# Kernel optimization log

Measured on AMD Instinct MI355X. Metric: run time of the kernel, lower is better.

The kernel has to match this reference:

```python
import jax, jax.numpy as jnp
import numpy as np

N, E = 100000, 1600000
F_IN, H, HG, L, C = 128, 128, 128, 3, 40


def setup_inputs() -> dict:
    key = jax.random.key(0)
    ks = jax.random.split(key, 12)
    s = 0.05
    return dict(
        x=jax.random.normal(ks[0], (N, F_IN), jnp.float32),
        edge_index=jax.random.randint(ks[1], (2, E), 0, N),
        edge_weight=jax.random.uniform(ks[2], (E,), jnp.float32),
        h0=jax.random.normal(ks[3], (N, HG), jnp.float32),
        linW=jax.random.normal(ks[4], (F_IN, H), jnp.float32) * s,
        linB=jnp.zeros((H,), jnp.float32),
        convW=jax.random.normal(ks[5], (L, H, H), jnp.float32) * s,
        convB=jnp.zeros((L, H), jnp.float32),
        gru_Wih=jax.random.normal(ks[6], (3 * HG, H), jnp.float32) * s,
        gru_Whh=jax.random.normal(ks[7], (3 * HG, HG), jnp.float32) * s,
        gru_bih=jnp.zeros((3 * HG,), jnp.float32),
        gru_bhh=jnp.zeros((3 * HG,), jnp.float32),
        fcW=jax.random.normal(ks[8], (HG, C), jnp.float32) * s,
        fcB=jnp.zeros((C,), jnp.float32),
    )


def _gru(x, h, Wih, Whh, bih, bhh):
    # torch.nn.GRUCell math (gate order: r, z, n)
    gi = x @ Wih.T + bih  # [N, 3*HG]
    gh = h @ Whh.T + bhh  # [N, 3*HG]
    ir, iz, in_ = jnp.split(gi, 3, axis=-1)
    hr, hz, hn = jnp.split(gh, 3, axis=-1)
    r = jax.nn.sigmoid(ir + hr)
    z = jax.nn.sigmoid(iz + hz)
    n = jnp.tanh(in_ + r * hn)
    return (1.0 - z) * n + z * h


def _gcn_conv(x, src, dst, ew, W, b, n_nodes):
    # PyG GCNConv: linear -> symmetric-normalized sparse aggregation -> bias
    xw = x @ W  # [N, H]
    deg = jax.ops.segment_sum(ew, dst, num_segments=n_nodes)
    dinv = jnp.where(deg > 0, jax.lax.rsqrt(deg), 0.0)
    norm = dinv[src] * ew * dinv[dst]  # [E+N]
    msg = xw[src] * norm[:, None]      # gather + scale (irregular access)
    out = jax.ops.segment_sum(msg, dst, num_segments=n_nodes)  # scatter-add
    return out + b


def reference(x, edge_index, edge_weight, h0, linW, linB, convW, convB,
              gru_Wih, gru_Whh, gru_bih, gru_bhh, fcW, fcB):
    n_nodes = x.shape[0]
    # GCNConv default: add self-loops with weight 1 before normalization
    loops = jnp.arange(n_nodes)
    src = jnp.concatenate([edge_index[0], loops])
    dst = jnp.concatenate([edge_index[1], loops])
    ew = jnp.concatenate([edge_weight, jnp.ones((n_nodes,), edge_weight.dtype)])

    h = h0
    xh = jax.nn.relu(x @ linW + linB)
    h = _gru(xh, h, gru_Wih, gru_Whh, gru_bih, gru_bhh)
    for l in range(convW.shape[0]):  # fixed small layer count
        xh = jax.nn.relu(_gcn_conv(xh, src, dst, ew, convW[l], convB[l], n_nodes))
        h = _gru(xh, h, gru_Wih, gru_Whh, gru_bih, gru_bhh)
    return h @ fcW + fcB
```

## Files before the change

### kernel.cpp

```cpp
#include <hip/hip_runtime.h>
#include <hip/hip_bf16.h>
#include <math.h>

typedef __attribute__((ext_vector_type(8))) short bf8_t;
typedef __attribute__((ext_vector_type(4))) float f4_t;
typedef __attribute__((ext_vector_type(8))) unsigned short us8_t;

__device__ inline unsigned short f2bf(float f) {
  union { float f; unsigned u; } x; x.f = f;
  unsigned r = x.u + 0x7FFF + ((x.u >> 16) & 1);
  return (unsigned short)(r >> 16);
}
__device__ inline float bflo(unsigned v) {
  union { unsigned u; float f; } x; x.u = v << 16; return x.f;
}
__device__ inline float bfhi(unsigned v) {
  union { unsigned u; float f; } x; x.u = v & 0xFFFF0000u; return x.f;
}

__device__ inline void async_copy16(const void* g, void* l) {
  __builtin_amdgcn_global_load_lds(
      (const __attribute__((address_space(1))) unsigned int*)g,
      (__attribute__((address_space(3))) unsigned int*)l, 16, 0, 0);
}


__device__ inline void packB_body(const float* __restrict__ W,
                                  unsigned short* __restrict__ out,
                                  int K, int Ncols, int ldw, int trans, int bid) {
  int idx = bid * 256 + threadIdx.x;
  int total = (Ncols / 16) * (K / 32) * 64;
  if (idx >= total) return;
  int lane = idx & 63;
  int frag = idx >> 6;
  int kt = K / 32;
  int k0 = frag % kt;
  int n0 = frag / kt;
  int n = n0 * 16 + (lane & 15);
  int kbase = k0 * 32 + (lane >> 4) * 8;
  us8_t v;
#pragma unroll
  for (int j = 0; j < 8; ++j) {
    int k = kbase + j;
    float f = trans ? W[(size_t)n * ldw + k] : W[(size_t)k * ldw + n];
    v[j] = f2bf(f);
  }
  *(us8_t*)(out + (size_t)idx * 8) = v;
}

__device__ inline void fill_body(const int* __restrict__ src, const int* __restrict__ dst,
                                 const float* __restrict__ ew, const int* __restrict__ rowptr,
                                 const int* __restrict__ pos, int2* __restrict__ csr,
                                 int E, int bid) {
  int e = bid * 256 + threadIdx.x;
  if (e >= E) return;
  int d = dst[e];
  int p = rowptr[d] + pos[e];
  unsigned long long v = (unsigned long long)(unsigned)src[e] |
                         ((unsigned long long)(unsigned)__float_as_int(ew[e]) << 32);
  __builtin_nontemporal_store(v, (unsigned long long*)(csr + p));
}

__device__ inline void deg_body(const int* __restrict__ rowptr, const int2* __restrict__ csr,
                                float* __restrict__ dinv, int N, int bid) {
  int n = bid * 256 + threadIdx.x;
  if (n >= N) return;
  int b = rowptr[n], e = rowptr[n + 1];
  float s = 1.0f;
  for (int j = b; j < e; ++j) {
    unsigned long long v = __builtin_nontemporal_load((const unsigned long long*)(csr + j));
    s += __int_as_float((int)(v >> 32));
  }
  dinv[n] = rsqrtf(s);
}

__device__ inline void norm_body(const int* __restrict__ rowptr, int2* __restrict__ csr,
                                 const float* __restrict__ dinv, int N, int bid) {
  int n = bid * 256 + threadIdx.x;
  if (n >= N) return;
  int b = rowptr[n], e = rowptr[n + 1];
  float dn = dinv[n];
  for (int j = b; j < e; ++j) {
    unsigned long long v = __builtin_nontemporal_load((const unsigned long long*)(csr + j));
    int s = (int)v;
    float w = dinv[s] * __int_as_float((int)(v >> 32)) * dn;
    unsigned long long nv = (unsigned long long)(unsigned)s |
                            ((unsigned long long)(unsigned)__float_as_int(w) << 32);
    __builtin_nontemporal_store(nv, (unsigned long long*)(csr + j));
  }
}

__device__ inline void gemm_body(const unsigned short* __restrict__ A,
                                 const unsigned short* __restrict__ Bp,
                                 const float* __restrict__ bias,
                                 unsigned short* __restrict__ C, int M, int bid,
                                 bool relu, bool hasbias, unsigned char* smem) {
  int wave = threadIdx.x >> 6, lane = threadIdx.x & 63;
  int row0 = (bid * 4 + wave) * 16;
  int m = lane & 15, q = lane >> 4;

#pragma unroll
  for (int i = 0; i < 8; ++i) {
    int f = wave * 8 + i;
    async_copy16((const unsigned char*)Bp + (size_t)f * 1024 + lane * 16,
                 smem + f * 1024);
  }
  __syncthreads();
  if (row0 >= M) return;

  int arow = row0 + m; if (arow >= M) arow = M - 1;
  bf8_t a[4];
#pragma unroll
  for (int k0 = 0; k0 < 4; ++k0)
    a[k0] = *(const bf8_t*)(A + (size_t)arow * 128 + k0 * 32 + q * 8);

#pragma unroll
  for (int n0 = 0; n0 < 8; ++n0) {
    f4_t acc = {};
#pragma unroll
    for (int k0 = 0; k0 < 4; ++k0) {
      bf8_t b = *(const bf8_t*)(smem + (n0 * 4 + k0) * 1024 + lane * 16);
      acc = __builtin_amdgcn_mfma_f32_16x16x32_bf16(a[k0], b, acc, 0, 0, 0);
    }
    int col = n0 * 16 + m;
    float bs = hasbias ? bias[col] : 0.f;
#pragma unroll
    for (int r = 0; r < 4; ++r) {
      int grow = row0 + q * 4 + r;
      if (grow < M) {
        float v = acc[r] + bs;
        if (relu) v = fmaxf(v, 0.f);
        C[(size_t)grow * 128 + col] = f2bf(v);
      }
    }
  }
}

__device__ inline void gru_stage(const unsigned short* __restrict__ Bi,
                                 const unsigned short* __restrict__ Bh,
                                 unsigned char* smem, int wave, int lane, int g) {
#pragma unroll
  for (int s = 0; s < 6; ++s) {
    int cc = g + 8 * (s >= 3 ? s - 3 : s);
    const unsigned short* src = (s < 3) ? Bi : Bh;
    int f = s * 4 + wave;
    async_copy16((const unsigned char*)src + ((size_t)(cc * 4 + wave)) * 1024 + lane * 16,
                 smem + f * 1024);
  }
}

__device__ inline void gru_core(const bf8_t* ax, const float* h_in, float* h_out,
                                const unsigned short* __restrict__ Bi,
                                const unsigned short* __restrict__ Bh,
                                const float* __restrict__ bih, const float* __restrict__ bhh,
                                int M, int row0, int wave, int lane, unsigned char* smem) {
  int m = lane & 15, q = lane >> 4;
  int arow = row0 + m; if (arow >= M) arow = M - 1;

  bf8_t ah[4];
#pragma unroll
  for (int k0 = 0; k0 < 4; ++k0) {
    const float* hp = h_in + (size_t)arow * 128 + k0 * 32 + q * 8;
    float4 h0 = *(const float4*)hp;
    float4 h1 = *(const float4*)(hp + 4);
    bf8_t t;
    t[0] = (short)f2bf(h0.x); t[1] = (short)f2bf(h0.y);
    t[2] = (short)f2bf(h0.z); t[3] = (short)f2bf(h0.w);
    t[4] = (short)f2bf(h1.x); t[5] = (short)f2bf(h1.y);
    t[6] = (short)f2bf(h1.z); t[7] = (short)f2bf(h1.w);
    ah[k0] = t;
  }

  for (int g = 0; g < 8; ++g) {
    __syncthreads();
    f4_t air = {}, aiz = {}, ain = {}, ahr = {}, ahz = {}, ahn = {};
#pragma unroll
    for (int k0 = 0; k0 < 4; ++k0) {
      bf8_t br = *(const bf8_t*)(smem + (0 * 4 + k0) * 1024 + lane * 16);
      bf8_t bz = *(const bf8_t*)(smem + (1 * 4 + k0) * 1024 + lane * 16);
      bf8_t bn = *(const bf8_t*)(smem + (2 * 4 + k0) * 1024 + lane * 16);
      bf8_t cr = *(const bf8_t*)(smem + (3 * 4 + k0) * 1024 + lane * 16);
      bf8_t cz = *(const bf8_t*)(smem + (4 * 4 + k0) * 1024 + lane * 16);
      bf8_t cn = *(const bf8_t*)(smem + (5 * 4 + k0) * 1024 + lane * 16);
      air = __builtin_amdgcn_mfma_f32_16x16x32_bf16(ax[k0], br, air, 0, 0, 0);
      aiz = __builtin_amdgcn_mfma_f32_16x16x32_bf16(ax[k0], bz, aiz, 0, 0, 0);
      ain = __builtin_amdgcn_mfma_f32_16x16x32_bf16(ax[k0], bn, ain, 0, 0, 0);
      ahr = __builtin_amdgcn_mfma_f32_16x16x32_bf16(ah[k0], cr, ahr, 0, 0, 0);
      ahz = __builtin_amdgcn_mfma_f32_16x16x32_bf16(ah[k0], cz, ahz, 0, 0, 0);
      ahn = __builtin_amdgcn_mfma_f32_16x16x32_bf16(ah[k0], cn, ahn, 0, 0, 0);
    }
    __syncthreads();
    if (g < 7) gru_stage(Bi, Bh, smem, wave, lane, g + 1);

    int col = g * 16 + m;
    float bir_ = bih[col], biz_ = bih[col + 128], bin_ = bih[col + 256];
    float bhr_ = bhh[col], bhz_ = bhh[col + 128], bhn_ = bhh[col + 256];
#pragma unroll
    for (int r = 0; r < 4; ++r) {
      int grow = row0 + q * 4 + r;
      if (grow < M) {
        float hprev = h_in[(size_t)grow * 128 + col];
        float rr = 1.f / (1.f + expf(-(air[r] + bir_ + ahr[r] + bhr_)));
        float zz = 1.f / (1.f + expf(-(aiz[r] + biz_ + ahz[r] + bhz_)));
        float nn = tanhf(ain[r] + bin_ + rr * (ahn[r] + bhn_));
        h_out[(size_t)grow * 128 + col] = (1.f - zz) * nn + zz * hprev;
      }
    }
  }
}

__device__ inline void gru_body(const unsigned short* __restrict__ xh,
                                const float* h_in, float* h_out,
                                const unsigned short* __restrict__ Bi,
                                const unsigned short* __restrict__ Bh,
                                const float* __restrict__ bih, const float* __restrict__ bhh,
                                int M, int bid, unsigned char* smem) {
  int wave = threadIdx.x >> 6, lane = threadIdx.x & 63;
  int row0 = (bid * 4 + wave) * 16;
  gru_stage(Bi, Bh, smem, wave, lane, 0);
  int m = lane & 15, q = lane >> 4;
  int arow = row0 + m; if (arow >= M) arow = M - 1;
  bf8_t ax[4];
#pragma unroll
  for (int k0 = 0; k0 < 4; ++k0)
    ax[k0] = *(const bf8_t*)(xh + (size_t)arow * 128 + k0 * 32 + q * 8);
  gru_core(ax, h_in, h_out, Bi, Bh, bih, bhh, M, row0, wave, lane, smem);
}


__global__ __launch_bounds__(256) void k_prep(
    const float* __restrict__ linW, const float* __restrict__ convW,
    const float* __restrict__ Wih, const float* __restrict__ Whh,
    unsigned short* __restrict__ linWp, unsigned short* __restrict__ convWp,
    unsigned short* __restrict__ Bi, unsigned short* __restrict__ Bh,
    int* __restrict__ cnt, int N) {
  int b = blockIdx.x;
  if (b < 8)  { packB_body(linW, linWp, 128, 128, 128, 0, b); return; }
  if (b < 32) { int l = (b - 8) >> 3;
                packB_body(convW + (size_t)l * 16384, convWp + (size_t)l * 16384,
                           128, 128, 128, 0, (b - 8) & 7); return; }
  if (b < 56) { packB_body(Wih, Bi, 128, 384, 128, 1, b - 32); return; }
  if (b < 80) { packB_body(Whh, Bh, 128, 384, 128, 1, b - 56); return; }
  int i = (b - 80) * 256 + threadIdx.x;
  if (i < N) cnt[i] = 0;
}

__global__ __launch_bounds__(256) void k_count_f2bf(
    const int* __restrict__ dst, int* __restrict__ cnt, int* __restrict__ pos, int E,
    const float* __restrict__ xin, unsigned short* __restrict__ xout, size_t n8,
    int nCnt) {
  if ((int)blockIdx.x < nCnt) {
    int e = blockIdx.x * 256 + threadIdx.x;
    if (e < E) pos[e] = atomicAdd(&cnt[dst[e]], 1);
    return;
  }
  size_t i = (size_t)(blockIdx.x - nCnt) * 256 + threadIdx.x;
  if (i >= n8) return;
  const float4* p = (const float4*)(xin + i * 8);
  float4 a = p[0], b = p[1];
  us8_t v;
  v[0] = f2bf(a.x); v[1] = f2bf(a.y); v[2] = f2bf(a.z); v[3] = f2bf(a.w);
  v[4] = f2bf(b.x); v[5] = f2bf(b.y); v[6] = f2bf(b.z); v[7] = f2bf(b.w);
  *(us8_t*)(xout + i * 8) = v;
}

__global__ __launch_bounds__(256) void k_scan_block(
    const int* __restrict__ cnt, int* __restrict__ partial,
    int* __restrict__ bsum, int n) {
  __shared__ int s[256];
  int tid = threadIdx.x;
  int i = blockIdx.x * 256 + tid;
  s[tid] = (i < n) ? cnt[i] : 0;
  __syncthreads();
#pragma unroll
  for (int d = 1; d < 256; d <<= 1) {
    int t = (tid >= d) ? s[tid - d] : 0;
    __syncthreads();
    s[tid] += t;
    __syncthreads();
  }
  if (i < n) partial[i] = s[tid];
  if (tid == 255) bsum[blockIdx.x] = s[255];
}

__global__ __launch_bounds__(512) void k_scan_sums(int* __restrict__ bsum, int nb) {
  __shared__ int s[512];
  int tid = threadIdx.x;
  s[tid] = (tid < nb) ? bsum[tid] : 0;
  __syncthreads();
#pragma unroll
  for (int d = 1; d < 512; d <<= 1) {
    int t = (tid >= d) ? s[tid - d] : 0;
    __syncthreads();
    s[tid] += t;
    __syncthreads();
  }
  if (tid < nb) bsum[tid] = s[tid];
}

__global__ __launch_bounds__(256) void k_scan_add(
    const int* __restrict__ partial, const int* __restrict__ bsum,
    int* __restrict__ rowptr, int n) {
  int i = blockIdx.x * 256 + threadIdx.x;
  if (i == 0) rowptr[0] = 0;
  if (i < n) {
    int v = partial[i] + (blockIdx.x > 0 ? bsum[blockIdx.x - 1] : 0);
    rowptr[i + 1] = v;
  }
}

__global__ __launch_bounds__(256) void k_fill_lin(
    const int* __restrict__ src, const int* __restrict__ dstI,
    const float* __restrict__ ew, const int* __restrict__ rowptr,
    const int* __restrict__ pos, int2* __restrict__ csr, int E,
    const unsigned short* __restrict__ A, const unsigned short* __restrict__ Bp,
    const float* __restrict__ bias, unsigned short* __restrict__ C, int M,
    int nFill) {
  __shared__ unsigned char smem[32 * 1024];
  if ((int)blockIdx.x < nFill) {
    fill_body(src, dstI, ew, rowptr, pos, csr, E, blockIdx.x);
    return;
  }
  gemm_body(A, Bp, bias, C, M, blockIdx.x - nFill, true, true, smem);
}

__global__ __launch_bounds__(256) void k_deg_gru(
    const int* __restrict__ rowptr, const int2* __restrict__ csr,
    float* __restrict__ dinv, int N,
    const unsigned short* __restrict__ xh, const float* h_in, float* h_out,
    const unsigned short* __restrict__ Bi, const unsigned short* __restrict__ Bh,
    const float* __restrict__ bih, const float* __restrict__ bhh, int M,
    int nDeg) {
  __shared__ unsigned char smem[24 * 1024];
  if ((int)blockIdx.x < nDeg) {
    deg_body(rowptr, csr, dinv, N, blockIdx.x);
    return;
  }
  gru_body(xh, h_in, h_out, Bi, Bh, bih, bhh, M, blockIdx.x - nDeg, smem);
}

__global__ __launch_bounds__(256) void k_norm_conv(
    const int* __restrict__ rowptr, int2* __restrict__ csr,
    const float* __restrict__ dinv, int N,
    const unsigned short* __restrict__ A, const unsigned short* __restrict__ Bp,
    unsigned short* __restrict__ C, int M, int nNorm) {
  __shared__ unsigned char smem[32 * 1024];
  if ((int)blockIdx.x < nNorm) {
    norm_body(rowptr, csr, dinv, N, blockIdx.x);
    return;
  }
  gemm_body(A, Bp, nullptr, C, M, blockIdx.x - nNorm, false, false, smem);
}

__global__ __launch_bounds__(256) void k_gru_conv(
    const unsigned short* __restrict__ xh, const float* h_in, float* h_out,
    const unsigned short* __restrict__ Bi, const unsigned short* __restrict__ Bh,
    const float* __restrict__ bih, const float* __restrict__ bhh,
    const unsigned short* __restrict__ Bp, unsigned short* __restrict__ xw,
    int M, int nGru) {
  __shared__ unsigned char smem[32 * 1024];
  if ((int)blockIdx.x < nGru) {
    gru_body(xh, h_in, h_out, Bi, Bh, bih, bhh, M, blockIdx.x, smem);
    return;
  }
  gemm_body(xh, Bp, nullptr, xw, M, blockIdx.x - nGru, false, false, smem);
}

__global__ __launch_bounds__(256) void k_gru(
    const unsigned short* __restrict__ xh, const float* h_in, float* h_out,
    const unsigned short* __restrict__ Bi, const unsigned short* __restrict__ Bh,
    const float* __restrict__ bih, const float* __restrict__ bhh, int M) {
  __shared__ unsigned char smem[24 * 1024];
  gru_body(xh, h_in, h_out, Bi, Bh, bih, bhh, M, blockIdx.x, smem);
}


__global__ __launch_bounds__(256) void k_gather(
    const int* __restrict__ rowptr, const int2* __restrict__ csr,
    const unsigned* __restrict__ xw,
    const float* __restrict__ dinv, const float* __restrict__ bias,
    unsigned* __restrict__ out, int N) {
  int wave = threadIdx.x >> 6;
  int lane = threadIdx.x & 63;
  int node = __builtin_amdgcn_readfirstlane(blockIdx.x * 4 + wave);
  if (node >= N) return;
  int beg = __builtin_amdgcn_readfirstlane(rowptr[node]);
  int end = __builtin_amdgcn_readfirstlane(rowptr[node + 1]);

  float accl = 0.f, acch = 0.f;
  int k = beg;
  for (; k + 4 <= end; k += 4) {
    unsigned long long r0 = __builtin_nontemporal_load((const unsigned long long*)(csr + k));
    unsigned long long r1 = __builtin_nontemporal_load((const unsigned long long*)(csr + k + 1));
    unsigned long long r2 = __builtin_nontemporal_load((const unsigned long long*)(csr + k + 2));
    unsigned long long r3 = __builtin_nontemporal_load((const unsigned long long*)(csr + k + 3));
    unsigned v0 = xw[((size_t)(unsigned)r0 << 6) + lane];
    unsigned v1 = xw[((size_t)(unsigned)r1 << 6) + lane];
    unsigned v2 = xw[((size_t)(unsigned)r2 << 6) + lane];
    unsigned v3 = xw[((size_t)(unsigned)r3 << 6) + lane];
    float w0 = __int_as_float((int)(r0 >> 32)), w1 = __int_as_float((int)(r1 >> 32));
    float w2 = __int_as_float((int)(r2 >> 32)), w3 = __int_as_float((int)(r3 >> 32));
    accl += bflo(v0) * w0; acch += bfhi(v0) * w0;
    accl += bflo(v1) * w1; acch += bfhi(v1) * w1;
    accl += bflo(v2) * w2; acch += bfhi(v2) * w2;
    accl += bflo(v3) * w3; acch += bfhi(v3) * w3;
  }
  for (; k < end; ++k) {
    unsigned long long r = __builtin_nontemporal_load((const unsigned long long*)(csr + k));
    unsigned v = xw[((size_t)(unsigned)r << 6) + lane];
    float w = __int_as_float((int)(r >> 32));
    accl += bflo(v) * w; acch += bfhi(v) * w;
  }

  float di = dinv[node];
  float sn = di * di;
  unsigned vs = xw[((size_t)node << 6) + lane];
  float2 b = *(const float2*)(bias + lane * 2);
  float rl = fmaxf(accl + bflo(vs) * sn + b.x, 0.f);
  float rh = fmaxf(acch + bfhi(vs) * sn + b.y, 0.f);
  unsigned o = (unsigned)f2bf(rl) | ((unsigned)f2bf(rh) << 16);
  out[((size_t)node << 6) + lane] = o;
}


template<bool RELU, bool BIAS>
__global__ __launch_bounds__(256) void k_gemm128(
    const float* __restrict__ A, const float* __restrict__ B,
    const float* __restrict__ bias, float* __restrict__ C, int M, int Nc) {
  __shared__ float As[64][36];
  __shared__ float Bs[32][64];
  int tid = threadIdx.x;
  int tx = tid & 15, ty = tid >> 4;
  int row0 = blockIdx.y * 64, col0 = blockIdx.x * 64;
  float acc[4][4] = {};

  for (int k0 = 0; k0 < 128; k0 += 32) {
#pragma unroll
    for (int i = 0; i < 2; ++i) {
      int f = tid + i * 256;
      int r = f >> 3, c4 = f & 7;
      int gr = row0 + r;
      float4 v = make_float4(0.f, 0.f, 0.f, 0.f);
      if (gr < M) v = *(const float4*)(A + (size_t)gr * 128 + k0 + c4 * 4);
      *(float4*)(&As[r][c4 * 4]) = v;
    }
#pragma unroll
    for (int i = 0; i < 2; ++i) {
      int f = tid + i * 256;
      int r = f >> 4, c4 = f & 15;
      int gc = col0 + c4 * 4;
      float4 v = make_float4(0.f, 0.f, 0.f, 0.f);
      if (gc + 3 < Nc) v = *(const float4*)(B + (size_t)(k0 + r) * Nc + gc);
      *(float4*)(&Bs[r][c4 * 4]) = v;
    }
    __syncthreads();
#pragma unroll
    for (int kk = 0; kk < 32; ++kk) {
      float4 b = *(float4*)(&Bs[kk][tx * 4]);
      float a0 = As[ty * 4 + 0][kk];
      float a1 = As[ty * 4 + 1][kk];
      float a2 = As[ty * 4 + 2][kk];
      float a3 = As[ty * 4 + 3][kk];
      acc[0][0] += a0 * b.x; acc[0][1] += a0 * b.y; acc[0][2] += a0 * b.z; acc[0][3] += a0 * b.w;
      acc[1][0] += a1 * b.x; acc[1][1] += a1 * b.y; acc[1][2] += a1 * b.z; acc[1][3] += a1 * b.w;
      acc[2][0] += a2 * b.x; acc[2][1] += a2 * b.y; acc[2][2] += a2 * b.z; acc[2][3] += a2 * b.w;
      acc[3][0] += a3 * b.x; acc[3][1] += a3 * b.y; acc[3][2] += a3 * b.z; acc[3][3] += a3 * b.w;
    }
    __syncthreads();
  }

#pragma unroll
  for (int i = 0; i < 4; ++i) {
    int gr = row0 + ty * 4 + i;
    if (gr >= M) continue;
#pragma unroll
    for (int j = 0; j < 4; ++j) {
      int gc = col0 + tx * 4 + j;
      if (gc >= Nc) continue;
      float v = acc[i][j];
      if (BIAS) v += bias[gc];
      if (RELU) v = fmaxf(v, 0.f);
      C[(size_t)gr * Nc + gc] = v;
    }
  }
}


extern "C" void kernel_launch(void* const* d_in, const int* in_sizes, int n_in,
                              void* d_out, int out_size, void* d_ws, size_t ws_size,
                              hipStream_t stream) {
  const float* x    = (const float*)d_in[0];
  const int*   ei   = (const int*)d_in[1];
  const float* ew   = (const float*)d_in[2];
  const float* h0   = (const float*)d_in[3];
  const float* linW = (const float*)d_in[4];
  const float* linB = (const float*)d_in[5];
  const float* convW= (const float*)d_in[6];
  const float* convB= (const float*)d_in[7];
  const float* Wih  = (const float*)d_in[8];
  const float* Whh  = (const float*)d_in[9];
  const float* bih  = (const float*)d_in[10];
  const float* bhh  = (const float*)d_in[11];
  const float* fcW  = (const float*)d_in[12];
  const float* fcB  = (const float*)d_in[13];

  int N = in_sizes[0] / 128;
  int E = in_sizes[1] / 2;
  const int* srcI = ei;
  const int* dstI = ei + E;
  int nb = (N + 255) / 256;

  float* ws = (float*)d_ws;
  size_t off = 0;
  float* dinv = ws + off; off += (size_t)N;
  if (off & 1) off++;
  float* h    = ws + off; off += (size_t)N * 128;
  int* iws = (int*)(ws + off);
  size_t ioff = 0;
  int2* csr    = (int2*)iws; ioff += (size_t)2 * E;
  int* cnt     = iws + ioff; ioff += (size_t)N;
  int* partial = iws + ioff; ioff += (size_t)N;
  int* bsum    = iws + ioff; ioff += 512;
  int* rowptr  = iws + ioff; ioff += (size_t)N + 1;
  ioff = (ioff + 3) & ~(size_t)3;
  unsigned short* usws = (unsigned short*)(iws + ioff);
  size_t uoff = 0;
  unsigned short* x_bf   = usws + uoff; uoff += (size_t)N * 128;
  unsigned short* xh_bf  = usws + uoff; uoff += (size_t)N * 128;
  unsigned short* xw_bf  = usws + uoff; uoff += (size_t)N * 128;
  unsigned short* linWp  = usws + uoff; uoff += 128 * 128;
  unsigned short* convWp = usws + uoff; uoff += 3 * 128 * 128;
  unsigned short* Bi     = usws + uoff; uoff += 384 * 128;
  unsigned short* Bh     = usws + uoff; uoff += 384 * 128;

  int* pos = (int*)xw_bf;

  int gwave = (N + 63) / 64;
  int nCnt  = (E + 255) / 256;
  int nF2   = (int)(((size_t)N * 16 + 255) / 256);

  k_prep<<<80 + nb, 256, 0, stream>>>(linW, convW, Wih, Whh,
                                      linWp, convWp, Bi, Bh, cnt, N);
  k_count_f2bf<<<nCnt + nF2, 256, 0, stream>>>(dstI, cnt, pos, E,
                                               x, x_bf, (size_t)N * 16, nCnt);
  k_scan_block<<<nb, 256, 0, stream>>>(cnt, partial, bsum, N);
  k_scan_sums<<<1, 512, 0, stream>>>(bsum, nb);
  k_scan_add<<<nb, 256, 0, stream>>>(partial, bsum, rowptr, N);
  k_fill_lin<<<nCnt + gwave, 256, 0, stream>>>(srcI, dstI, ew, rowptr, pos, csr, E,
                                               x_bf, linWp, linB, xh_bf, N, nCnt);
  k_deg_gru<<<nb + gwave, 256, 0, stream>>>(rowptr, csr, dinv, N,
                                            xh_bf, h0, h, Bi, Bh, bih, bhh, N, nb);
  k_norm_conv<<<nb + gwave, 256, 0, stream>>>(rowptr, csr, dinv, N,
                                              xh_bf, convWp, xw_bf, N, nb);

  int ggat = (N + 3) / 4;
  k_gather<<<ggat, 256, 0, stream>>>(rowptr, csr, (const unsigned*)xw_bf, dinv,
                                     convB, (unsigned*)xh_bf, N);
  k_gru_conv<<<2 * gwave, 256, 0, stream>>>(
      xh_bf, h, h, Bi, Bh, bih, bhh,
      convWp + (size_t)1 * 128 * 128, xw_bf, N, gwave);
  k_gather<<<ggat, 256, 0, stream>>>(rowptr, csr, (const unsigned*)xw_bf, dinv,
                                     convB + 128, (unsigned*)xh_bf, N);
  k_gru_conv<<<2 * gwave, 256, 0, stream>>>(
      xh_bf, h, h, Bi, Bh, bih, bhh,
      convWp + (size_t)2 * 128 * 128, xw_bf, N, gwave);
  k_gather<<<ggat, 256, 0, stream>>>(rowptr, csr, (const unsigned*)xw_bf, dinv,
                                     convB + 256, (unsigned*)xh_bf, N);
  k_gru<<<gwave, 256, 0, stream>>>(xh_bf, h, h, Bi, Bh, bih, bhh, N);
  dim3 g40(1, (N + 63) / 64);
  k_gemm128<false, true><<<g40, 256, 0, stream>>>(h, fcW, fcB, (float*)d_out, N, 40);
}
```

Baseline: 976.9 us.

## Use 512-thread blocks for fused GEMM/GRU kernels and fast sigmoid/tanh

The fused fill/deg/norm and GEMM/GRU kernels move from 256 to 512 threads per block, so each block covers 128 rows. The LDS weight staging is then split across 8 waves, which halves the per-block copy work and the number of redundant weight loads across the grid. The GRU gate math now uses __expf plus a hardware reciprocal instead of expf, 1/x and tanhf, trading some accuracy for fewer instructions. Larger blocks and launch_bounds(512,4) may also change register allocation and occupancy.

```diff
diff --git a/kernel.cpp b/kernel.cpp
--- a/kernel.cpp
+++ b/kernel.cpp
@@ -16,6 +16,12 @@
 }
 __device__ inline float bfhi(unsigned v) {
   union { unsigned u; float f; } x; x.u = v & 0xFFFF0000u; return x.f;
+}
+__device__ inline float fast_sig(float x) {
+  return __builtin_amdgcn_rcpf(1.f + __expf(-x));
+}
+__device__ inline float fast_tanh(float x) {
+  return 1.f - 2.f * __builtin_amdgcn_rcpf(1.f + __expf(2.f * x));
 }
 
 __device__ inline void async_copy16(const void* g, void* l) {
@@ -52,7 +58,7 @@
                                  const float* __restrict__ ew, const int* __restrict__ rowptr,
                                  const int* __restrict__ pos, int2* __restrict__ csr,
                                  int E, int bid) {
-  int e = bid * 256 + threadIdx.x;
+  int e = bid * 512 + threadIdx.x;
   if (e >= E) return;
   int d = dst[e];
   int p = rowptr[d] + pos[e];
@@ -63,7 +69,7 @@
 
 __device__ inline void deg_body(const int* __restrict__ rowptr, const int2* __restrict__ csr,
                                 float* __restrict__ dinv, int N, int bid) {
-  int n = bid * 256 + threadIdx.x;
+  int n = bid * 512 + threadIdx.x;
   if (n >= N) return;
   int b = rowptr[n], e = rowptr[n + 1];
   float s = 1.0f;
@@ -76,7 +82,7 @@
 
 __device__ inline void norm_body(const int* __restrict__ rowptr, int2* __restrict__ csr,
                                  const float* __restrict__ dinv, int N, int bid) {
-  int n = bid * 256 + threadIdx.x;
+  int n = bid * 512 + threadIdx.x;
   if (n >= N) return;
   int b = rowptr[n], e = rowptr[n + 1];
   float dn = dinv[n];
@@ -90,18 +96,18 @@
   }
 }
 
-__device__ inline void gemm_body(const unsigned short* __restrict__ A,
-                                 const unsigned short* __restrict__ Bp,
-                                 const float* __restrict__ bias,
-                                 unsigned short* __restrict__ C, int M, int bid,
-                                 bool relu, bool hasbias, unsigned char* smem) {
+__device__ inline void gemm_body8(const unsigned short* __restrict__ A,
+                                  const unsigned short* __restrict__ Bp,
+                                  const float* __restrict__ bias,
+                                  unsigned short* __restrict__ C, int M, int bid,
+                                  bool relu, bool hasbias, unsigned char* smem) {
   int wave = threadIdx.x >> 6, lane = threadIdx.x & 63;
-  int row0 = (bid * 4 + wave) * 16;
+  int row0 = (bid * 8 + wave) * 16;
   int m = lane & 15, q = lane >> 4;
 
 #pragma unroll
-  for (int i = 0; i < 8; ++i) {
-    int f = wave * 8 + i;
+  for (int i = 0; i < 4; ++i) {
+    int f = wave * 4 + i;
     async_copy16((const unsigned char*)Bp + (size_t)f * 1024 + lane * 16,
                  smem + f * 1024);
   }
@@ -136,15 +142,16 @@
   }
 }
 
-__device__ inline void gru_stage(const unsigned short* __restrict__ Bi,
-                                 const unsigned short* __restrict__ Bh,
-                                 unsigned char* smem, int wave, int lane, int g) {
-#pragma unroll
-  for (int s = 0; s < 6; ++s) {
+__device__ inline void gru_stage8(const unsigned short* __restrict__ Bi,
+                                  const unsigned short* __restrict__ Bh,
+                                  unsigned char* smem, int wave, int lane, int g) {
+#pragma unroll
+  for (int i = 0; i < 3; ++i) {
+    int f = wave * 3 + i;
+    int s = f >> 2, k0 = f & 3;
     int cc = g + 8 * (s >= 3 ? s - 3 : s);
     const unsigned short* src = (s < 3) ? Bi : Bh;
-    int f = s * 4 + wave;
-    async_copy16((const unsigned char*)src + ((size_t)(cc * 4 + wave)) * 1024 + lane * 16,
+    async_copy16((const unsigned char*)src + ((size_t)(cc * 4 + k0)) * 1024 + lane * 16,
                  smem + f * 1024);
   }
 }
@@ -190,7 +197,7 @@
       ahn = __builtin_amdgcn_mfma_f32_16x16x32_bf16(ah[k0], cn, ahn, 0, 0, 0);
     }
     __syncthreads();
-    if (g < 7) gru_stage(Bi, Bh, smem, wave, lane, g + 1);
+    if (g < 7) gru_stage8(Bi, Bh, smem, wave, lane, g + 1);
 
     int col = g * 16 + m;
     float bir_ = bih[col], biz_ = bih[col + 128], bin_ = bih[col + 256];
@@ -200,24 +207,24 @@
       int grow = row0 + q * 4 + r;
       if (grow < M) {
         float hprev = h_in[(size_t)grow * 128 + col];
-        float rr = 1.f / (1.f + expf(-(air[r] + bir_ + ahr[r] + bhr_)));
-        float zz = 1.f / (1.f + expf(-(aiz[r] + biz_ + ahz[r] + bhz_)));
-        float nn = tanhf(ain[r] + bin_ + rr * (ahn[r] + bhn_));
+        float rr = fast_sig(air[r] + bir_ + ahr[r] + bhr_);
+        float zz = fast_sig(aiz[r] + biz_ + ahz[r] + bhz_);
+        float nn = fast_tanh(ain[r] + bin_ + rr * (ahn[r] + bhn_));
         h_out[(size_t)grow * 128 + col] = (1.f - zz) * nn + zz * hprev;
       }
     }
   }
 }
 
-__device__ inline void gru_body(const unsigned short* __restrict__ xh,
-                                const float* h_in, float* h_out,
-                                const unsigned short* __restrict__ Bi,
-                                const unsigned short* __restrict__ Bh,
-                                const float* __restrict__ bih, const float* __restrict__ bhh,
-                                int M, int bid, unsigned char* smem) {
+__device__ inline void gru_body8(const unsigned short* __restrict__ xh,
+                                 const float* h_in, float* h_out,
+                                 const unsigned short* __restrict__ Bi,
+                                 const unsigned short* __restrict__ Bh,
+                                 const float* __restrict__ bih, const float* __restrict__ bhh,
+                                 int M, int bid, unsigned char* smem) {
   int wave = threadIdx.x >> 6, lane = threadIdx.x & 63;
-  int row0 = (bid * 4 + wave) * 16;
-  gru_stage(Bi, Bh, smem, wave, lane, 0);
+  int row0 = (bid * 8 + wave) * 16;
+  gru_stage8(Bi, Bh, smem, wave, lane, 0);
   int m = lane & 15, q = lane >> 4;
   int arow = row0 + m; if (arow >= M) arow = M - 1;
   bf8_t ax[4];
@@ -309,7 +316,7 @@
   }
 }
 
-__global__ __launch_bounds__(256) void k_fill_lin(
+__global__ __launch_bounds__(512, 4) void k_fill_lin(
     const int* __restrict__ src, const int* __restrict__ dstI,
     const float* __restrict__ ew, const int* __restrict__ rowptr,
     const int* __restrict__ pos, int2* __restrict__ csr, int E,
@@ -321,10 +328,10 @@
     fill_body(src, dstI, ew, rowptr, pos, csr, E, blockIdx.x);
     return;
   }
-  gemm_body(A, Bp, bias, C, M, blockIdx.x - nFill, true, true, smem);
-}
-
-__global__ __launch_bounds__(256) void k_deg_gru(
+  gemm_body8(A, Bp, bias, C, M, blockIdx.x - nFill, true, true, smem);
+}
+
+__global__ __launch_bounds__(512, 4) void k_deg_gru(
     const int* __restrict__ rowptr, const int2* __restrict__ csr,
     float* __restrict__ dinv, int N,
     const unsigned short* __restrict__ xh, const float* h_in, float* h_out,
@@ -336,10 +343,10 @@
     deg_body(rowptr, csr, dinv, N, blockIdx.x);
     return;
   }
-  gru_body(xh, h_in, h_out, Bi, Bh, bih, bhh, M, blockIdx.x - nDeg, smem);
-}
-
-__global__ __launch_bounds__(256) void k_norm_conv(
+  gru_body8(xh, h_in, h_out, Bi, Bh, bih, bhh, M, blockIdx.x - nDeg, smem);
+}
+
+__global__ __launch_bounds__(512, 4) void k_norm_conv(
     const int* __restrict__ rowptr, int2* __restrict__ csr,
     const float* __restrict__ dinv, int N,
     const unsigned short* __restrict__ A, const unsigned short* __restrict__ Bp,
@@ -349,10 +356,10 @@
     norm_body(rowptr, csr, dinv, N, blockIdx.x);
     return;
   }
-  gemm_body(A, Bp, nullptr, C, M, blockIdx.x - nNorm, false, false, smem);
-}
-
-__global__ __launch_bounds__(256) void k_gru_conv(
+  gemm_body8(A, Bp, nullptr, C, M, blockIdx.x - nNorm, false, false, smem);
+}
+
+__global__ __launch_bounds__(512, 4) void k_gru_conv(
     const unsigned short* __restrict__ xh, const float* h_in, float* h_out,
     const unsigned short* __restrict__ Bi, const unsigned short* __restrict__ Bh,
     const float* __restrict__ bih, const float* __restrict__ bhh,
@@ -360,18 +367,18 @@
     int M, int nGru) {
   __shared__ unsigned char smem[32 * 1024];
   if ((int)blockIdx.x < nGru) {
-    gru_body(xh, h_in, h_out, Bi, Bh, bih, bhh, M, blockIdx.x, smem);
+    gru_body8(xh, h_in, h_out, Bi, Bh, bih, bhh, M, blockIdx.x, smem);
     return;
   }
-  gemm_body(xh, Bp, nullptr, xw, M, blockIdx.x - nGru, false, false, smem);
-}
-
-__global__ __launch_bounds__(256) void k_gru(
+  gemm_body8(xh, Bp, nullptr, xw, M, blockIdx.x - nGru, false, false, smem);
+}
+
+__global__ __launch_bounds__(512, 4) void k_gru(
     const unsigned short* __restrict__ xh, const float* h_in, float* h_out,
     const unsigned short* __restrict__ Bi, const unsigned short* __restrict__ Bh,
     const float* __restrict__ bih, const float* __restrict__ bhh, int M) {
   __shared__ unsigned char smem[24 * 1024];
-  gru_body(xh, h_in, h_out, Bi, Bh, bih, bhh, M, blockIdx.x, smem);
+  gru_body8(xh, h_in, h_out, Bi, Bh, bih, bhh, M, blockIdx.x, smem);
 }
 
 
@@ -535,9 +542,11 @@
 
   int* pos = (int*)xw_bf;
 
-  int gwave = (N + 63) / 64;
-  int nCnt  = (E + 255) / 256;
-  int nF2   = (int)(((size_t)N * 16 + 255) / 256);
+  int gw8  = (N + 127) / 128;
+  int nCnt = (E + 255) / 256;
+  int nF2  = (int)(((size_t)N * 16 + 255) / 256);
+  int n512 = (N + 511) / 512;
+  int e512 = (E + 511) / 512;
 
   k_prep<<<80 + nb, 256, 0, stream>>>(linW, convW, Wih, Whh,
                                       linWp, convWp, Bi, Bh, cnt, N);
@@ -546,27 +555,27 @@
   k_scan_block<<<nb, 256, 0, stream>>>(cnt, partial, bsum, N);
   k_scan_sums<<<1, 512, 0, stream>>>(bsum, nb);
   k_scan_add<<<nb, 256, 0, stream>>>(partial, bsum, rowptr, N);
-  k_fill_lin<<<nCnt + gwave, 256, 0, stream>>>(srcI, dstI, ew, rowptr, pos, csr, E,
-                                               x_bf, linWp, linB, xh_bf, N, nCnt);
-  k_deg_gru<<<nb + gwave, 256, 0, stream>>>(rowptr, csr, dinv, N,
-                                            xh_bf, h0, h, Bi, Bh, bih, bhh, N, nb);
-  k_norm_conv<<<nb + gwave, 256, 0, stream>>>(rowptr, csr, dinv, N,
-                                              xh_bf, convWp, xw_bf, N, nb);
+  k_fill_lin<<<e512 + gw8, 512, 0, stream>>>(srcI, dstI, ew, rowptr, pos, csr, E,
+                                             x_bf, linWp, linB, xh_bf, N, e512);
+  k_deg_gru<<<n512 + gw8, 512, 0, stream>>>(rowptr, csr, dinv, N,
+                                            xh_bf, h0, h, Bi, Bh, bih, bhh, N, n512);
+  k_norm_conv<<<n512 + gw8, 512, 0, stream>>>(rowptr, csr, dinv, N,
+                                              xh_bf, convWp, xw_bf, N, n512);
 
   int ggat = (N + 3) / 4;
   k_gather<<<ggat, 256, 0, stream>>>(rowptr, csr, (const unsigned*)xw_bf, dinv,
                                      convB, (unsigned*)xh_bf, N);
-  k_gru_conv<<<2 * gwave, 256, 0, stream>>>(
+  k_gru_conv<<<2 * gw8, 512, 0, stream>>>(
       xh_bf, h, h, Bi, Bh, bih, bhh,
-      convWp + (size_t)1 * 128 * 128, xw_bf, N, gwave);
+      convWp + (size_t)1 * 128 * 128, xw_bf, N, gw8);
   k_gather<<<ggat, 256, 0, stream>>>(rowptr, csr, (const unsigned*)xw_bf, dinv,
                                      convB + 128, (unsigned*)xh_bf, N);
-  k_gru_conv<<<2 * gwave, 256, 0, stream>>>(
+  k_gru_conv<<<2 * gw8, 512, 0, stream>>>(
       xh_bf, h, h, Bi, Bh, bih, bhh,
-      convWp + (size_t)2 * 128 * 128, xw_bf, N, gwave);
+      convWp + (size_t)2 * 128 * 128, xw_bf, N, gw8);
   k_gather<<<ggat, 256, 0, stream>>>(rowptr, csr, (const unsigned*)xw_bf, dinv,
                                      convB + 256, (unsigned*)xh_bf, N);
-  k_gru<<<gwave, 256, 0, stream>>>(xh_bf, h, h, Bi, Bh, bih, bhh, N);
+  k_gru<<<gw8, 512, 0, stream>>>(xh_bf, h, h, Bi, Bh, bih, bhh, N);
   dim3 g40(1, (N + 63) / 64);
   k_gemm128<false, true><<<g40, 256, 0, stream>>>(h, fcW, fcB, (float*)d_out, N, 40);
 }
```

New measurement: 969.7 us. Within noise of the previous version (-0.7%).
